# Kernel optimization log

Hardware: AMD Instinct MI355X
Metric: run time of the kernel (lower is better)

## Reference

```python
import jax, jax.numpy as jnp
import numpy as np

N_NODES = 50000
N_EDGES = 500000
IN_FEAT = 128
OUT_FEAT = 128
N_REL = 16


def setup_inputs() -> dict:
    key = jax.random.key(0)
    k1, k2, k3, k4 = jax.random.split(key, 4)
    entity_embeddings = jax.random.normal(k1, (N_NODES, IN_FEAT), dtype=jnp.float32)
    # xavier_uniform over (in, out) fan per relation slice
    limit = (6.0 / (IN_FEAT + OUT_FEAT)) ** 0.5
    weight = jax.random.uniform(k2, (N_REL, IN_FEAT, OUT_FEAT), dtype=jnp.float32,
                                minval=-limit, maxval=limit)
    edge_index = jax.random.randint(k3, (2, N_EDGES), 0, N_NODES, dtype=jnp.int64)
    edge_type = jax.random.randint(k4, (N_EDGES,), 0, N_REL, dtype=jnp.int64)
    return {"entity_embeddings": entity_embeddings, "weight": weight,
            "edge_index": edge_index, "edge_type": edge_type}


def reference(entity_embeddings, weight, edge_index, edge_type):
    # RGCN message passing: for each edge e with relation r:
    #   msg_e = x[src_e] @ W[r];  out[tgt_e] += msg_e;  out = relu(out)
    # Vectorized: transform every node by every relation once (R*N*in*out flops),
    # then gather the (relation, src) slice per edge and scatter-add to tgt.
    # This avoids gathering a per-edge (E, in, out) weight tensor.
    num_entities = entity_embeddings.shape[0]
    src = edge_index[0]
    tgt = edge_index[1]
    transformed = jnp.einsum('ni,rio->rno', entity_embeddings, weight)  # (R, N, O)
    msg = transformed[edge_type, src]                                   # (E, O)
    messages = jax.ops.segment_sum(msg, tgt, num_segments=num_entities)  # (N, O)
    # Dropout is identity in eval mode; reference omits it (deterministic baseline).
    return jax.nn.relu(messages)
```

## Files before the change

### kernel.cpp

```cpp
#include <hip/hip_runtime.h>
#include <hip/hip_bf16.h>

typedef __attribute__((ext_vector_type(8))) __bf16 bf16x8;
typedef __attribute__((ext_vector_type(4))) __bf16 bf16x4;
typedef __attribute__((ext_vector_type(2))) __bf16 bf16x2;
typedef __attribute__((ext_vector_type(4))) float f32x4;

#define IN_FEAT 128
#define OUT_FEAT 128
#define N_REL 16
#define TILE_M 64

__global__ void cvtX_kernel(const float* __restrict__ x, __bf16* __restrict__ xb, int n) {
    int i = (blockIdx.x * blockDim.x + threadIdx.x) * 4;
    if (i < n) {
        float4 v = *(const float4*)(x + i);
        bf16x4 o = { (__bf16)v.x, (__bf16)v.y, (__bf16)v.z, (__bf16)v.w };
        *(bf16x4*)(xb + i) = o;
    }
}

__global__ __launch_bounds__(256) void prep_kernel(
        const float* __restrict__ w, __bf16* __restrict__ wt,
        const int* __restrict__ etype, const int* __restrict__ etgt, int n,
        int* __restrict__ cnt_rel, int* __restrict__ cnt_tgt) {
    __shared__ __bf16 tile[32 * 136];
    __shared__ int h[N_REL];
    int t = threadIdx.x;
    if (blockIdx.x < 64) {
        int r = blockIdx.x >> 2;
        int n0 = (blockIdx.x & 3) * 32;
        const float* W = w + (size_t)r * IN_FEAT * OUT_FEAT;
        __bf16* T = wt + (size_t)r * IN_FEAT * OUT_FEAT;
        #pragma unroll
        for (int it = 0; it < 16; ++it) {
            int idx = t + it * 256;
            int k = idx >> 5, dn = idx & 31;
            tile[dn * 136 + k] = (__bf16)W[k * OUT_FEAT + n0 + dn];
        }
        __syncthreads();
        #pragma unroll
        for (int it = 0; it < 2; ++it) {
            int idx = t + it * 256;
            int nn = idx >> 4, c = idx & 15;
            bf16x8 v = *(const bf16x8*)(&tile[nn * 136 + c * 8]);
            *(bf16x8*)(T + (size_t)(n0 + nn) * IN_FEAT + c * 8) = v;
        }
    } else {
        if (t < N_REL) h[t] = 0;
        __syncthreads();
        int stride = (gridDim.x - 64) * blockDim.x;
        for (int i = (blockIdx.x - 64) * blockDim.x + t; i < n; i += stride) {
            atomicAdd(&h[etype[i]], 1);
            atomicAdd(&cnt_tgt[etgt[i]], 1);
        }
        __syncthreads();
        if (t < N_REL) atomicAdd(&cnt_rel[t], h[t]);
    }
}

__global__ void hist_kernel(const int* __restrict__ etype, int n, int* __restrict__ cnt_rel) {
    __shared__ int h[N_REL];
    if (threadIdx.x < N_REL) h[threadIdx.x] = 0;
    __syncthreads();
    for (int i = blockIdx.x * blockDim.x + threadIdx.x; i < n; i += gridDim.x * blockDim.x)
        atomicAdd(&h[etype[i]], 1);
    __syncthreads();
    if (threadIdx.x < N_REL) atomicAdd(&cnt_rel[threadIdx.x], h[threadIdx.x]);
}
__global__ void prefix_kernel(const int* __restrict__ cnt, int* __restrict__ meta) {
    if (threadIdx.x == 0) {
        int off = 0, toff = 0;
        for (int r = 0; r < N_REL; ++r) {
            meta[r] = off; meta[32 + r] = toff; meta[64 + r] = off;
            off += cnt[r];
            toff += (cnt[r] + TILE_M - 1) / TILE_M;
        }
        meta[16] = off; meta[48] = toff;
    }
}

__global__ void scanA_kernel(const int* __restrict__ cnt, int n, int* __restrict__ partial) {
    __shared__ int s[256];
    int i = blockIdx.x * 256 + threadIdx.x;
    s[threadIdx.x] = (i < n) ? cnt[i] : 0;
    __syncthreads();
    for (int off = 128; off > 0; off >>= 1) {
        if (threadIdx.x < off) s[threadIdx.x] += s[threadIdx.x + off];
        __syncthreads();
    }
    if (threadIdx.x == 0) partial[blockIdx.x] = s[0];
}
__global__ void scanBP_kernel(int* __restrict__ partial, int nchunks,
                              const int* __restrict__ cnt_rel, int* __restrict__ meta) {
    __shared__ int s[256];
    int t = threadIdx.x;
    int v = (t < nchunks) ? partial[t] : 0;
    s[t] = v;
    __syncthreads();
    for (int off = 1; off < 256; off <<= 1) {
        int x = (t >= off) ? s[t - off] : 0;
        __syncthreads();
        s[t] += x;
        __syncthreads();
    }
    if (t < nchunks) partial[t] = s[t] - v;
    if (t == 0) {
        int off = 0, toff = 0;
        for (int r = 0; r < N_REL; ++r) {
            meta[r] = off; meta[32 + r] = toff; meta[64 + r] = off;
            off += cnt_rel[r];
            toff += (cnt_rel[r] + TILE_M - 1) / TILE_M;
        }
        meta[16] = off; meta[48] = toff;
    }
}
__global__ void scanC_kernel(const int* __restrict__ cnt, int n, const int* __restrict__ partial,
                             int* __restrict__ base, int* __restrict__ cursor) {
    __shared__ int s[256];
    int t = threadIdx.x, i = blockIdx.x * 256 + t;
    int v = (i < n) ? cnt[i] : 0;
    s[t] = v;
    __syncthreads();
    for (int off = 1; off < 256; off <<= 1) {
        int x = (t >= off) ? s[t - off] : 0;
        __syncthreads();
        s[t] += x;
        __syncthreads();
    }
    int b = partial[blockIdx.x] + s[t] - v;
    if (i < n) { base[i] = b; cursor[i] = b; }
}

#define SCATTER_EPT 2
#define SCATTER_CHUNK (256 * SCATTER_EPT)
__global__ __launch_bounds__(256) void scatter_slot_kernel(
        const int* __restrict__ esrc, const int* __restrict__ etgt,
        const int* __restrict__ etype, int n,
        int* __restrict__ cursor_rel, int* __restrict__ cursor_tgt,
        int* __restrict__ bsrc, int* __restrict__ bslot) {
    __shared__ int lcnt[N_REL];
    __shared__ int lbase[N_REL];
    int t = threadIdx.x;
    if (t < N_REL) lcnt[t] = 0;
    __syncthreads();
    int base = blockIdx.x * SCATTER_CHUNK;
    int rj[SCATTER_EPT], offj[SCATTER_EPT];
    #pragma unroll
    for (int j = 0; j < SCATTER_EPT; ++j) {
        int i = base + j * 256 + t;
        if (i < n) {
            int r = etype[i];
            rj[j] = r;
            offj[j] = atomicAdd(&lcnt[r], 1);
        } else rj[j] = -1;
    }
    __syncthreads();
    if (t < N_REL) lbase[t] = atomicAdd(&cursor_rel[t], lcnt[t]);
    __syncthreads();
    #pragma unroll
    for (int j = 0; j < SCATTER_EPT; ++j) {
        if (rj[j] >= 0) {
            int i = base + j * 256 + t;
            int p = lbase[rj[j]] + offj[j];
            bsrc[p] = esrc[i];
            bslot[p] = atomicAdd(&cursor_tgt[etgt[i]], 1);
        }
    }
}

__global__ __launch_bounds__(256) void scatter_kernel(
        const int* __restrict__ esrc, const int* __restrict__ etgt,
        const int* __restrict__ etype, int n,
        int* __restrict__ cursor,
        int* __restrict__ bsrc, int* __restrict__ btgt) {
    __shared__ int lcnt[N_REL];
    __shared__ int lbase[N_REL];
    int t = threadIdx.x;
    if (t < N_REL) lcnt[t] = 0;
    __syncthreads();
    int base = blockIdx.x * SCATTER_CHUNK;
    int rj[SCATTER_EPT], offj[SCATTER_EPT];
    #pragma unroll
    for (int j = 0; j < SCATTER_EPT; ++j) {
        int i = base + j * 256 + t;
        if (i < n) {
            int r = etype[i];
            rj[j] = r;
            offj[j] = atomicAdd(&lcnt[r], 1);
        } else rj[j] = -1;
    }
    __syncthreads();
    if (t < N_REL) lbase[t] = atomicAdd(&cursor[t], lcnt[t]);
    __syncthreads();
    #pragma unroll
    for (int j = 0; j < SCATTER_EPT; ++j) {
        if (rj[j] >= 0) {
            int i = base + j * 256 + t;
            int p = lbase[rj[j]] + offj[j];
            bsrc[p] = esrc[i];
            btgt[p] = etgt[i];
        }
    }
}

__global__ __launch_bounds__(256) void gemm_msg5_kernel(
    const float* __restrict__ X,
    const __bf16* __restrict__ Wt,
    const int* __restrict__ bsrc, const int* __restrict__ bslot,
    const int* __restrict__ meta,
    __bf16* __restrict__ msg) {
    __shared__ __align__(16) __bf16 Bs[OUT_FEAT * 128];
    __shared__ __align__(16) __bf16 As[TILE_M * 128];
    __shared__ int s_slot[TILE_M];

    int bid = blockIdx.x;
    const int* rel_off = meta;
    const int* tile_pre = meta + 32;
    if (bid >= tile_pre[16]) return;
    int rel = 0;
    while (bid >= tile_pre[rel + 1]) rel++;
    int tile = bid - tile_pre[rel];
    int row_start = rel_off[rel] + tile * TILE_M;
    int m_valid = min(TILE_M, rel_off[rel + 1] - row_start);

    int tid = threadIdx.x;
    uint4* BsV = (uint4*)Bs;
    bf16x8* AsV = (bf16x8*)As;
    const bf16x8* AsF = (const bf16x8*)As;
    const bf16x8* BsF = (const bf16x8*)Bs;

    {
        const __bf16* wsrc = Wt + (size_t)rel * IN_FEAT * OUT_FEAT;
        #pragma unroll
        for (int i = 0; i < 8; ++i) {
            int cid = tid + i * 256;
            int row = cid >> 4, c = cid & 15;
            int feat = (row & 15) * 8 + (row >> 4);
            uint4 v = *(const uint4*)(wsrc + (size_t)feat * IN_FEAT + c * 8);
            BsV[row * 16 + (c ^ (row & 15))] = v;
        }
    }
    {
        #pragma unroll
        for (int i = 0; i < 4; ++i) {
            int cid = tid + i * 256;
            int r = cid >> 4, c = cid & 15;
            int srcn = (r < m_valid) ? bsrc[row_start + r] : 0;
            const float4* xr = (const float4*)(X + (size_t)srcn * IN_FEAT + c * 8);
            float4 f0 = xr[0], f1 = xr[1];
            bf16x8 o = { (__bf16)f0.x, (__bf16)f0.y, (__bf16)f0.z, (__bf16)f0.w,
                         (__bf16)f1.x, (__bf16)f1.y, (__bf16)f1.z, (__bf16)f1.w };
            AsV[r * 16 + (c ^ (r & 15))] = o;
        }
        if (tid < TILE_M) s_slot[tid] = (tid < m_valid) ? bslot[row_start + tid] : -1;
    }
    __syncthreads();

    int wave = tid >> 6, lane = tid & 63;
    int q = lane >> 4, ln = lane & 15;

    f32x4 acc[8];
    f32x4 z = { 0.f, 0.f, 0.f, 0.f };
    #pragma unroll
    for (int nf = 0; nf < 8; ++nf) acc[nf] = z;

    int myrow = wave * 16 + ln;
    #pragma unroll
    for (int kk = 0; kk < 4; ++kk) {
        bf16x8 a = AsF[myrow * 16 + ((kk * 4 + q) ^ ln)];
        #pragma unroll
        for (int nf = 0; nf < 8; ++nf) {
            bf16x8 b = BsF[(nf * 16 + ln) * 16 + ((kk * 4 + q) ^ ln)];
            acc[nf] = __builtin_amdgcn_mfma_f32_16x16x32_bf16(a, b, acc[nf], 0, 0, 0);
        }
    }

    #pragma unroll
    for (int reg = 0; reg < 4; ++reg) {
        int row = wave * 16 + q * 4 + reg;
        int slot = s_slot[row];
        if (slot >= 0) {
            bf16x8 o = { (__bf16)acc[0][reg], (__bf16)acc[1][reg],
                         (__bf16)acc[2][reg], (__bf16)acc[3][reg],
                         (__bf16)acc[4][reg], (__bf16)acc[5][reg],
                         (__bf16)acc[6][reg], (__bf16)acc[7][reg] };
            *(bf16x8*)(msg + (size_t)slot * OUT_FEAT + ln * 8) = o;
        }
    }
}

__global__ __launch_bounds__(256) void segsum2_kernel(
        const __bf16* __restrict__ msg, const int* __restrict__ base,
        int nnodes, int ntot, float* __restrict__ out) {
    int n = blockIdx.x * 4 + (threadIdx.x >> 6);
    if (n >= nnodes) return;
    int l = threadIdx.x & 63;
    int half = l >> 5, cl = l & 31;
    int s0 = base[n];
    int s1 = (n == nnodes - 1) ? ntot : base[n + 1];
    float4 a = { 0.f, 0.f, 0.f, 0.f };
    int s = s0;
    for (; s + 2 <= s1; s += 2) {
        bf16x4 m = *(const bf16x4*)(msg + (size_t)(s + half) * OUT_FEAT + cl * 4);
        a.x += (float)m[0]; a.y += (float)m[1]; a.z += (float)m[2]; a.w += (float)m[3];
    }
    if (s < s1 && half == 0) {
        bf16x4 m = *(const bf16x4*)(msg + (size_t)s * OUT_FEAT + cl * 4);
        a.x += (float)m[0]; a.y += (float)m[1]; a.z += (float)m[2]; a.w += (float)m[3];
    }
    a.x += __shfl_xor(a.x, 32, 64);
    a.y += __shfl_xor(a.y, 32, 64);
    a.z += __shfl_xor(a.z, 32, 64);
    a.w += __shfl_xor(a.w, 32, 64);
    if (half == 0) {
        float4 o = { fmaxf(a.x, 0.f), fmaxf(a.y, 0.f), fmaxf(a.z, 0.f), fmaxf(a.w, 0.f) };
        *(float4*)(out + (size_t)n * OUT_FEAT + cl * 4) = o;
    }
}

#define LDA 136
__global__ __launch_bounds__(256) void gemm_scatter_kernel(
    const __bf16* __restrict__ Xb, const __bf16* __restrict__ Wt,
    const int* __restrict__ bsrc, const int* __restrict__ btgt,
    const int* __restrict__ meta, float* __restrict__ out) {
    __shared__ __align__(16) __bf16 As2[TILE_M * LDA];
    __shared__ __align__(16) __bf16 Bs2[OUT_FEAT * LDA];
    __shared__ int s_tgt[TILE_M];
    int bid = blockIdx.x;
    const int* rel_off = meta;
    const int* tile_pre = meta + 32;
    if (bid >= tile_pre[16]) return;
    int rel = 0;
    while (bid >= tile_pre[rel + 1]) rel++;
    int tile = bid - tile_pre[rel];
    int row_start = rel_off[rel] + tile * TILE_M;
    int m_valid = min(TILE_M, rel_off[rel + 1] - row_start);
    int t = threadIdx.x;
    {
        const __bf16* src = Wt + rel * IN_FEAT * OUT_FEAT;
        #pragma unroll
        for (int i = 0; i < 8; ++i) {
            int cid = t + i * 256;
            int n = cid >> 4, c = cid & 15;
            uint4 v = *(const uint4*)(src + n * IN_FEAT + c * 8);
            *(uint4*)(&Bs2[n * LDA + c * 8]) = v;
        }
    }
    {
        #pragma unroll
        for (int i = 0; i < 4; ++i) {
            int cid = t + i * 256;
            int r = cid >> 4, c = cid & 15;
            int srcn = (r < m_valid) ? bsrc[row_start + r] : 0;
            uint4 v = *(const uint4*)(Xb + srcn * IN_FEAT + c * 8);
            *(uint4*)(&As2[r * LDA + c * 8]) = v;
        }
        if (t < TILE_M) s_tgt[t] = (t < m_valid) ? btgt[row_start + t] : -1;
    }
    __syncthreads();
    int wave = t >> 6, lane = t & 63;
    int q = lane >> 4, ln = lane & 15;
    f32x4 acc[8];
    f32x4 z = { 0.f, 0.f, 0.f, 0.f };
    #pragma unroll
    for (int nf = 0; nf < 8; ++nf) acc[nf] = z;
    #pragma unroll
    for (int kk = 0; kk < 4; ++kk) {
        bf16x8 a = *(const bf16x8*)(&As2[(wave * 16 + ln) * LDA + kk * 32 + q * 8]);
        #pragma unroll
        for (int nf = 0; nf < 8; ++nf) {
            bf16x8 b = *(const bf16x8*)(&Bs2[(nf * 16 + ln) * LDA + kk * 32 + q * 8]);
            acc[nf] = __builtin_amdgcn_mfma_f32_16x16x32_bf16(a, b, acc[nf], 0, 0, 0);
        }
    }
    #pragma unroll
    for (int reg = 0; reg < 4; ++reg) {
        int r = wave * 16 + q * 4 + reg;
        int tgt = s_tgt[r];
        if (tgt >= 0) {
            float* orow = out + (size_t)tgt * OUT_FEAT + ln;
            #pragma unroll
            for (int nf = 0; nf < 8; ++nf)
                unsafeAtomicAdd(orow + nf * 16, acc[nf][reg]);
        }
    }
}

__global__ void relu_kernel(float* __restrict__ out, int n) {
    int i = (blockIdx.x * blockDim.x + threadIdx.x) * 4;
    if (i < n) {
        float4 v = *(float4*)(out + i);
        v.x = fmaxf(v.x, 0.f); v.y = fmaxf(v.y, 0.f);
        v.z = fmaxf(v.z, 0.f); v.w = fmaxf(v.w, 0.f);
        *(float4*)(out + i) = v;
    }
}

extern "C" void kernel_launch(void* const* d_in, const int* in_sizes, int n_in,
                              void* d_out, int out_size, void* d_ws, size_t ws_size,
                              hipStream_t stream) {
    const float* x = (const float*)d_in[0];
    const float* w = (const float*)d_in[1];
    const int* eidx = (const int*)d_in[2];
    const int* etype = (const int*)d_in[3];
    const int E = in_sizes[3];
    const int nX = in_sizes[0];
    const int N = out_size / OUT_FEAT;
    const int* esrc = eidx;
    const int* etgt = eidx + E;
    float* out = (float*)d_out;

    char* ws = (char*)d_ws;
    size_t off = 0;
    auto alloc = [&](size_t sz) { size_t o = off; off = (off + sz + 255) & ~(size_t)255; return o; };
    size_t off_Xb   = alloc((size_t)nX * 2);
    size_t off_Wt   = alloc((size_t)N_REL * IN_FEAT * OUT_FEAT * 2);
    size_t off_cnt  = alloc(64);
    size_t off_meta = alloc(512);
    size_t off_bsrc = alloc((size_t)E * 4);
    size_t off_bsl  = alloc((size_t)E * 4);
    size_t off_ctgt = alloc((size_t)(N + 16) * 4);
    size_t off_cur  = alloc((size_t)N * 4);
    size_t off_base = alloc((size_t)N * 4);
    size_t off_part = alloc(1024);
    size_t off_msg  = alloc((size_t)E * OUT_FEAT * 2);
    bool big = (ws_size >= off);

    __bf16* Xb = (__bf16*)(ws + off_Xb);
    __bf16* Wt = (__bf16*)(ws + off_Wt);
    int* meta  = (int*)(ws + off_meta);
    int* bsrc  = (int*)(ws + off_bsrc);
    int* bsl   = (int*)(ws + off_bsl);

    int scatter_blocks = (E + SCATTER_CHUNK - 1) / SCATTER_CHUNK;
    int max_tiles = (E + TILE_M - 1) / TILE_M + N_REL;

    if (big) {
        int* cnt_tgt = (int*)(ws + off_ctgt);
        int* cnt_rel = cnt_tgt + N;
        int* cursor  = (int*)(ws + off_cur);
        int* base    = (int*)(ws + off_base);
        int* partial = (int*)(ws + off_part);
        __bf16* msg  = (__bf16*)(ws + off_msg);
        int nchunks = (N + 255) / 256;

        hipMemsetAsync(cnt_tgt, 0, (size_t)(N + 16) * 4, stream);
        prep_kernel<<<64 + 1024, 256, 0, stream>>>(w, Wt, etype, etgt, E, cnt_rel, cnt_tgt);
        scanA_kernel<<<nchunks, 256, 0, stream>>>(cnt_tgt, N, partial);
        scanBP_kernel<<<1, 256, 0, stream>>>(partial, nchunks, cnt_rel, meta);
        scanC_kernel<<<nchunks, 256, 0, stream>>>(cnt_tgt, N, partial, base, cursor);
        scatter_slot_kernel<<<scatter_blocks, 256, 0, stream>>>(
            esrc, etgt, etype, E, meta + 64, cursor, bsrc, bsl);
        gemm_msg5_kernel<<<max_tiles, 256, 0, stream>>>(x, Wt, bsrc, bsl, meta, msg);
        segsum2_kernel<<<(N + 3) / 4, 256, 0, stream>>>(msg, base, N, E, out);
    } else {
        int* cnt = (int*)(ws + off_cnt);
        hipMemsetAsync(cnt, 0, 64, stream);
        hipMemsetAsync(out, 0, (size_t)out_size * 4, stream);
        cvtX_kernel<<<(nX / 4 + 255) / 256, 256, 0, stream>>>(x, Xb, nX);
        prep_kernel<<<64, 256, 0, stream>>>(w, Wt, etype, etgt, E, cnt, nullptr);
        hist_kernel<<<1024, 256, 0, stream>>>(etype, E, cnt);
        prefix_kernel<<<1, 64, 0, stream>>>(cnt, meta);
        scatter_kernel<<<scatter_blocks, 256, 0, stream>>>(
            esrc, etgt, etype, E, meta + 64, bsrc, bsl);
        gemm_scatter_kernel<<<max_tiles, 256, 0, stream>>>(Xb, Wt, bsrc, bsl, meta, out);
        relu_kernel<<<(out_size / 4 + 255) / 256, 256, 0, stream>>>(out, out_size);
    }
}
```

Before: 236.0 us.

## Pre-convert X to bf16 in prep, merge scan kernels, widen segment-sum loads

Converts the node embeddings to bf16 once inside the prep kernel using extra blocks, so the message GEMM gathers half-width rows instead of converting fp32 per edge. The two-pass partial scan and final scan are merged into one kernel, where each block reduces the preceding partials itself, removing one launch. The segment-sum kernel now has four edge groups per node reading 8 bf16 each, reduced with shuffles. This adds a bf16 copy of X to the workspace and redundant partial sums per scan block.

```diff
diff --git a/kernel.cpp b/kernel.cpp
--- a/kernel.cpp
+++ b/kernel.cpp
@@ -3,7 +3,6 @@
 
 typedef __attribute__((ext_vector_type(8))) __bf16 bf16x8;
 typedef __attribute__((ext_vector_type(4))) __bf16 bf16x4;
-typedef __attribute__((ext_vector_type(2))) __bf16 bf16x2;
 typedef __attribute__((ext_vector_type(4))) float f32x4;
 
 #define IN_FEAT 128
@@ -11,17 +10,9 @@
 #define N_REL 16
 #define TILE_M 64
 
-__global__ void cvtX_kernel(const float* __restrict__ x, __bf16* __restrict__ xb, int n) {
-    int i = (blockIdx.x * blockDim.x + threadIdx.x) * 4;
-    if (i < n) {
-        float4 v = *(const float4*)(x + i);
-        bf16x4 o = { (__bf16)v.x, (__bf16)v.y, (__bf16)v.z, (__bf16)v.w };
-        *(bf16x4*)(xb + i) = o;
-    }
-}
-
 __global__ __launch_bounds__(256) void prep_kernel(
         const float* __restrict__ w, __bf16* __restrict__ wt,
+        const float* __restrict__ x, __bf16* __restrict__ xb, int nX, int cvtb,
         const int* __restrict__ etype, const int* __restrict__ etgt, int n,
         int* __restrict__ cnt_rel, int* __restrict__ cnt_tgt) {
     __shared__ __bf16 tile[32 * 136];
@@ -46,11 +37,20 @@
             bf16x8 v = *(const bf16x8*)(&tile[nn * 136 + c * 8]);
             *(bf16x8*)(T + (size_t)(n0 + nn) * IN_FEAT + c * 8) = v;
         }
+    } else if (blockIdx.x < 64 + cvtb) {
+        int i = ((blockIdx.x - 64) * 256 + t) * 8;
+        if (i < nX) {
+            const float4* xr = (const float4*)(x + i);
+            float4 f0 = xr[0], f1 = xr[1];
+            bf16x8 o = { (__bf16)f0.x, (__bf16)f0.y, (__bf16)f0.z, (__bf16)f0.w,
+                         (__bf16)f1.x, (__bf16)f1.y, (__bf16)f1.z, (__bf16)f1.w };
+            *(bf16x8*)(xb + i) = o;
+        }
     } else {
         if (t < N_REL) h[t] = 0;
         __syncthreads();
-        int stride = (gridDim.x - 64) * blockDim.x;
-        for (int i = (blockIdx.x - 64) * blockDim.x + t; i < n; i += stride) {
+        int stride = (gridDim.x - 64 - cvtb) * blockDim.x;
+        for (int i = (blockIdx.x - 64 - cvtb) * blockDim.x + t; i < n; i += stride) {
             atomicAdd(&h[etype[i]], 1);
             atomicAdd(&cnt_tgt[etgt[i]], 1);
         }
@@ -91,11 +91,27 @@
     }
     if (threadIdx.x == 0) partial[blockIdx.x] = s[0];
 }
-__global__ void scanBP_kernel(int* __restrict__ partial, int nchunks,
-                              const int* __restrict__ cnt_rel, int* __restrict__ meta) {
+__global__ void scanC2_kernel(const int* __restrict__ cnt, int n,
+                              const int* __restrict__ partial,
+                              const int* __restrict__ cnt_rel, int* __restrict__ meta,
+                              int* __restrict__ base, int* __restrict__ cursor) {
     __shared__ int s[256];
+    __shared__ int sbase;
     int t = threadIdx.x;
-    int v = (t < nchunks) ? partial[t] : 0;
+    int pb = 0;
+    for (int i = t; i < (int)blockIdx.x; i += 256) pb += partial[i];
+    s[t] = pb;
+    __syncthreads();
+    for (int off = 128; off > 0; off >>= 1) {
+        if (t < off) s[t] += s[t + off];
+        __syncthreads();
+    }
+    if (t == 0) sbase = s[0];
+    __syncthreads();
+    int blockbase = sbase;
+    __syncthreads();
+    int i = blockIdx.x * 256 + t;
+    int v = (i < n) ? cnt[i] : 0;
     s[t] = v;
     __syncthreads();
     for (int off = 1; off < 256; off <<= 1) {
@@ -104,8 +120,9 @@
         s[t] += x;
         __syncthreads();
     }
-    if (t < nchunks) partial[t] = s[t] - v;
-    if (t == 0) {
+    int b = blockbase + s[t] - v;
+    if (i < n) { base[i] = b; cursor[i] = b; }
+    if (blockIdx.x == 0 && t == 0) {
         int off = 0, toff = 0;
         for (int r = 0; r < N_REL; ++r) {
             meta[r] = off; meta[32 + r] = toff; meta[64 + r] = off;
@@ -114,22 +131,6 @@
         }
         meta[16] = off; meta[48] = toff;
     }
-}
-__global__ void scanC_kernel(const int* __restrict__ cnt, int n, const int* __restrict__ partial,
-                             int* __restrict__ base, int* __restrict__ cursor) {
-    __shared__ int s[256];
-    int t = threadIdx.x, i = blockIdx.x * 256 + t;
-    int v = (i < n) ? cnt[i] : 0;
-    s[t] = v;
-    __syncthreads();
-    for (int off = 1; off < 256; off <<= 1) {
-        int x = (t >= off) ? s[t - off] : 0;
-        __syncthreads();
-        s[t] += x;
-        __syncthreads();
-    }
-    int b = partial[blockIdx.x] + s[t] - v;
-    if (i < n) { base[i] = b; cursor[i] = b; }
 }
 
 #define SCATTER_EPT 2
@@ -204,8 +205,8 @@
     }
 }
 
-__global__ __launch_bounds__(256) void gemm_msg5_kernel(
-    const float* __restrict__ X,
+__global__ __launch_bounds__(256) void gemm_msg6_kernel(
+    const __bf16* __restrict__ Xb,
     const __bf16* __restrict__ Wt,
     const int* __restrict__ bsrc, const int* __restrict__ bslot,
     const int* __restrict__ meta,
@@ -226,7 +227,7 @@
 
     int tid = threadIdx.x;
     uint4* BsV = (uint4*)Bs;
-    bf16x8* AsV = (bf16x8*)As;
+    uint4* AsV = (uint4*)As;
     const bf16x8* AsF = (const bf16x8*)As;
     const bf16x8* BsF = (const bf16x8*)Bs;
 
@@ -247,11 +248,8 @@
             int cid = tid + i * 256;
             int r = cid >> 4, c = cid & 15;
             int srcn = (r < m_valid) ? bsrc[row_start + r] : 0;
-            const float4* xr = (const float4*)(X + (size_t)srcn * IN_FEAT + c * 8);
-            float4 f0 = xr[0], f1 = xr[1];
-            bf16x8 o = { (__bf16)f0.x, (__bf16)f0.y, (__bf16)f0.z, (__bf16)f0.w,
-                         (__bf16)f1.x, (__bf16)f1.y, (__bf16)f1.z, (__bf16)f1.w };
-            AsV[r * 16 + (c ^ (r & 15))] = o;
+            uint4 v = *(const uint4*)(Xb + (size_t)srcn * IN_FEAT + c * 8);
+            AsV[r * 16 + (c ^ (r & 15))] = v;
         }
         if (tid < TILE_M) s_slot[tid] = (tid < m_valid) ? bslot[row_start + tid] : -1;
     }
@@ -290,35 +288,43 @@
     }
 }
 
-__global__ __launch_bounds__(256) void segsum2_kernel(
+__global__ __launch_bounds__(256) void segsum3_kernel(
         const __bf16* __restrict__ msg, const int* __restrict__ base,
         int nnodes, int ntot, float* __restrict__ out) {
     int n = blockIdx.x * 4 + (threadIdx.x >> 6);
     if (n >= nnodes) return;
     int l = threadIdx.x & 63;
-    int half = l >> 5, cl = l & 31;
+    int g = l >> 4, ln = l & 15;
     int s0 = base[n];
     int s1 = (n == nnodes - 1) ? ntot : base[n + 1];
-    float4 a = { 0.f, 0.f, 0.f, 0.f };
-    int s = s0;
-    for (; s + 2 <= s1; s += 2) {
-        bf16x4 m = *(const bf16x4*)(msg + (size_t)(s + half) * OUT_FEAT + cl * 4);
-        a.x += (float)m[0]; a.y += (float)m[1]; a.z += (float)m[2]; a.w += (float)m[3];
-    }
-    if (s < s1 && half == 0) {
-        bf16x4 m = *(const bf16x4*)(msg + (size_t)s * OUT_FEAT + cl * 4);
-        a.x += (float)m[0]; a.y += (float)m[1]; a.z += (float)m[2]; a.w += (float)m[3];
-    }
-    a.x += __shfl_xor(a.x, 32, 64);
-    a.y += __shfl_xor(a.y, 32, 64);
-    a.z += __shfl_xor(a.z, 32, 64);
-    a.w += __shfl_xor(a.w, 32, 64);
-    if (half == 0) {
-        float4 o = { fmaxf(a.x, 0.f), fmaxf(a.y, 0.f), fmaxf(a.z, 0.f), fmaxf(a.w, 0.f) };
-        *(float4*)(out + (size_t)n * OUT_FEAT + cl * 4) = o;
-    }
-}
-
+    float a[8] = { 0.f, 0.f, 0.f, 0.f, 0.f, 0.f, 0.f, 0.f };
+    for (int s = s0 + g; s < s1; s += 4) {
+        bf16x8 m = *(const bf16x8*)(msg + (size_t)s * OUT_FEAT + ln * 8);
+        #pragma unroll
+        for (int j = 0; j < 8; ++j) a[j] += (float)m[j];
+    }
+    #pragma unroll
+    for (int j = 0; j < 8; ++j) {
+        a[j] += __shfl_xor(a[j], 16, 64);
+        a[j] += __shfl_xor(a[j], 32, 64);
+    }
+    if (g == 0) {
+        float4 o0 = { fmaxf(a[0], 0.f), fmaxf(a[1], 0.f), fmaxf(a[2], 0.f), fmaxf(a[3], 0.f) };
+        float4 o1 = { fmaxf(a[4], 0.f), fmaxf(a[5], 0.f), fmaxf(a[6], 0.f), fmaxf(a[7], 0.f) };
+        float* dst = out + (size_t)n * OUT_FEAT + ln * 8;
+        *(float4*)dst = o0;
+        *(float4*)(dst + 4) = o1;
+    }
+}
+
+__global__ void cvtX_kernel(const float* __restrict__ x, __bf16* __restrict__ xb, int n) {
+    int i = (blockIdx.x * blockDim.x + threadIdx.x) * 4;
+    if (i < n) {
+        float4 v = *(const float4*)(x + i);
+        bf16x4 o = { (__bf16)v.x, (__bf16)v.y, (__bf16)v.z, (__bf16)v.w };
+        *(bf16x4*)(xb + i) = o;
+    }
+}
 #define LDA 136
 __global__ __launch_bounds__(256) void gemm_scatter_kernel(
     const __bf16* __restrict__ Xb, const __bf16* __restrict__ Wt,
@@ -386,7 +392,6 @@
         }
     }
 }
-
 __global__ void relu_kernel(float* __restrict__ out, int n) {
     int i = (blockIdx.x * blockDim.x + threadIdx.x) * 4;
     if (i < n) {
@@ -444,22 +449,23 @@
         int* partial = (int*)(ws + off_part);
         __bf16* msg  = (__bf16*)(ws + off_msg);
         int nchunks = (N + 255) / 256;
+        int cvtb = (nX / 8 + 255) / 256;
 
         hipMemsetAsync(cnt_tgt, 0, (size_t)(N + 16) * 4, stream);
-        prep_kernel<<<64 + 1024, 256, 0, stream>>>(w, Wt, etype, etgt, E, cnt_rel, cnt_tgt);
+        prep_kernel<<<64 + cvtb + 1024, 256, 0, stream>>>(
+            w, Wt, x, Xb, nX, cvtb, etype, etgt, E, cnt_rel, cnt_tgt);
         scanA_kernel<<<nchunks, 256, 0, stream>>>(cnt_tgt, N, partial);
-        scanBP_kernel<<<1, 256, 0, stream>>>(partial, nchunks, cnt_rel, meta);
-        scanC_kernel<<<nchunks, 256, 0, stream>>>(cnt_tgt, N, partial, base, cursor);
+        scanC2_kernel<<<nchunks, 256, 0, stream>>>(cnt_tgt, N, partial, cnt_rel, meta, base, cursor);
         scatter_slot_kernel<<<scatter_blocks, 256, 0, stream>>>(
             esrc, etgt, etype, E, meta + 64, cursor, bsrc, bsl);
-        gemm_msg5_kernel<<<max_tiles, 256, 0, stream>>>(x, Wt, bsrc, bsl, meta, msg);
-        segsum2_kernel<<<(N + 3) / 4, 256, 0, stream>>>(msg, base, N, E, out);
+        gemm_msg6_kernel<<<max_tiles, 256, 0, stream>>>(Xb, Wt, bsrc, bsl, meta, msg);
+        segsum3_kernel<<<(N + 3) / 4, 256, 0, stream>>>(msg, base, N, E, out);
     } else {
         int* cnt = (int*)(ws + off_cnt);
         hipMemsetAsync(cnt, 0, 64, stream);
         hipMemsetAsync(out, 0, (size_t)out_size * 4, stream);
         cvtX_kernel<<<(nX / 4 + 255) / 256, 256, 0, stream>>>(x, Xb, nX);
-        prep_kernel<<<64, 256, 0, stream>>>(w, Wt, etype, etgt, E, cnt, nullptr);
+        prep_kernel<<<64, 256, 0, stream>>>(w, Wt, x, Xb, 0, 0, etype, etgt, E, cnt, nullptr);
         hist_kernel<<<1024, 256, 0, stream>>>(etype, E, cnt);
         prefix_kernel<<<1, 64, 0, stream>>>(cnt, meta);
         scatter_kernel<<<scatter_blocks, 256, 0, stream>>>(
```

After: 225.9 us. 1.04x faster.
